# Performance work log

Hardware: AMD Instinct MI355X
Metric: run time of the kernel (lower is better)

Reference implementation:

```python
import jax, jax.numpy as jnp
import numpy as np

NUM_HEADS = 8
SPARSITY = 0.25
BOUNDARY_W = 0.5
LN_EPS = 1e-5


def setup_inputs() -> dict:
    key = jax.random.key(0)
    ks = jax.random.split(key, 16)
    B, C, H, W = 8, 256, 64, 64
    Ch = C // 4
    s = lambda *sh: 1.0 / np.sqrt(sh[-1])
    inp = {
        'x': jax.random.normal(ks[0], (B, C, H, W), jnp.float32),
        'boundary_map': jax.random.uniform(ks[1], (B, 1, H, W), jnp.float32),
        'imp_w1': jax.random.normal(ks[2], (Ch, C), jnp.float32) * s(C),
        'imp_b1': jnp.zeros((Ch,), jnp.float32),
        'imp_w2': jax.random.normal(ks[3], (1, Ch), jnp.float32) * s(Ch),
        'imp_b2': jnp.zeros((1,), jnp.float32),
        'wq': jax.random.normal(ks[4], (C, C), jnp.float32) * s(C),
        'bq': jnp.zeros((C,), jnp.float32),
        'wk': jax.random.normal(ks[5], (C, C), jnp.float32) * s(C),
        'bk': jnp.zeros((C,), jnp.float32),
        'wv': jax.random.normal(ks[6], (C, C), jnp.float32) * s(C),
        'bv': jnp.zeros((C,), jnp.float32),
        'wo': jax.random.normal(ks[7], (C, C), jnp.float32) * (0.1 * s(C)),
        'bo': jnp.zeros((C,), jnp.float32),
        'ln_g': jnp.ones((C,), jnp.float32),
        'ln_b': jnp.zeros((C,), jnp.float32),
    }
    return inp


def reference(x, boundary_map, imp_w1, imp_b1, imp_w2, imp_b2,
              wq, bq, wk, bk, wv, bv, wo, bo, ln_g, ln_b):
    B, C, H, W = x.shape
    N = H * W
    K = max(int(N * SPARSITY), 1)
    nh = NUM_HEADS
    hd = C // nh
    scale = hd ** -0.5

    # importance net: 1x1 conv -> GELU -> 1x1 conv -> sigmoid
    h = jnp.einsum('bchw,oc->bohw', x, imp_w1) + imp_b1[None, :, None, None]
    h = jax.nn.gelu(h, approximate=False)
    imp = jnp.einsum('bchw,oc->bohw', h, imp_w2) + imp_b2[None, :, None, None]
    importance = jax.nn.sigmoid(imp) + BOUNDARY_W * boundary_map  # [B,1,H,W]

    # top-K token selection
    _, top_idx = jax.lax.top_k(importance.reshape(B, N), K)  # [B,K]

    x_flat = x.transpose(0, 2, 3, 1).reshape(B, N, C)
    x_sp = jnp.take_along_axis(x_flat, top_idx[..., None], axis=1)  # [B,K,C]

    # sparse self-attention over K tokens
    q = (jnp.einsum('bkc,oc->bko', x_sp, wq) + bq).reshape(B, K, nh, hd)
    k = (jnp.einsum('bkc,oc->bko', x_sp, wk) + bk).reshape(B, K, nh, hd)
    v = (jnp.einsum('bkc,oc->bko', x_sp, wv) + bv).reshape(B, K, nh, hd)
    attn = jax.nn.softmax(jnp.einsum('bqhd,bkhd->bhqk', q, k) * scale, axis=-1)
    o = jnp.einsum('bhqk,bkhd->bqhd', attn, v).reshape(B, K, C)
    out_sp = jnp.einsum('bkc,oc->bko', o, wo) + bo

    # residual + LayerNorm
    y = out_sp + x_sp
    mu = jnp.mean(y, axis=-1, keepdims=True)
    var = jnp.mean(jnp.square(y - mu), axis=-1, keepdims=True)
    enh = (y - mu) * jax.lax.rsqrt(var + LN_EPS) * ln_g + ln_b  # [B,K,C]

    # scatter enhanced tokens back
    bidx = jnp.arange(B)[:, None]
    out_full = x_flat.at[bidx, top_idx].set(enh)
    out = out_full.reshape(B, H, W, C).transpose(0, 3, 1, 2)
    return out, importance
```

## Files before the change

kernel.cpp:

```cpp
#include <hip/hip_runtime.h>
#include <math.h>

#define B_ 8
#define C_ 256
#define N_ 4096
#define K_ 1024
#define NH_ 8
#define HD_ 32

typedef __attribute__((ext_vector_type(8))) short short8;
typedef __attribute__((ext_vector_type(8))) _Float16 half8;
typedef __attribute__((ext_vector_type(4))) _Float16 half4;
typedef __attribute__((ext_vector_type(4))) float f32x4;

#if __has_builtin(__builtin_amdgcn_exp2f)
#define EXPX(x) __builtin_amdgcn_exp2f(x)
#define QSCALE (0.17677669529663688f * 1.4426950408889634f)
#else
#define EXPX(x) __expf(x)
#define QSCALE 0.17677669529663688f
#endif

__device__ __forceinline__ unsigned bfr(float x){
  unsigned u = __float_as_uint(x);
  return (u + 0x7FFFu + ((u >> 16) & 1u)) >> 16;
}
__device__ __forceinline__ unsigned pk2(float lo, float hi){
  return bfr(lo) | (bfr(hi) << 16);
}
__device__ __forceinline__ unsigned hpk(float a, float b){
  _Float16 ha = (_Float16)a, hb = (_Float16)b;
  unsigned short ua = __builtin_bit_cast(unsigned short, ha);
  unsigned short ub = __builtin_bit_cast(unsigned short, hb);
  return (unsigned)ua | ((unsigned)ub << 16);
}
__device__ __forceinline__ half4 pk4rtz(float a, float b, float c, float d){
  auto lo = __builtin_amdgcn_cvt_pkrtz(a, b);
  auto hi = __builtin_amdgcn_cvt_pkrtz(c, d);
  uint2 u = make_uint2(__builtin_bit_cast(unsigned, lo), __builtin_bit_cast(unsigned, hi));
  return __builtin_bit_cast(half4, u);
}

__global__ __launch_bounds__(256) void w2h_kernel(
    const float* __restrict__ wq, const float* __restrict__ wk,
    const float* __restrict__ wv, const float* __restrict__ wo,
    unsigned short* __restrict__ wh)
{
  const float* src = blockIdx.y==0 ? wq : blockIdx.y==1 ? wk : blockIdx.y==2 ? wv : wo;
  const int e = (blockIdx.x*256 + threadIdx.x)*8;
  float4 a = *(const float4*)(src + e);
  float4 b = *(const float4*)(src + e + 4);
  uint4 o;
  o.x = hpk(a.x, a.y); o.y = hpk(a.z, a.w);
  o.z = hpk(b.x, b.y); o.w = hpk(b.z, b.w);
  *(uint4*)(wh + (size_t)blockIdx.y*65536 + e) = o;
}

__global__ __launch_bounds__(256) void imp_kernel(
    const float* __restrict__ x, const float* __restrict__ bmap,
    const float* __restrict__ w1, const float* __restrict__ b1,
    const float* __restrict__ w2, const float* __restrict__ b2,
    float* __restrict__ imp_out, float* __restrict__ outx)
{
  __shared__ float xs[64][256];
  const int t = threadIdx.x;
  const int b = blockIdx.x >> 6, tile = blockIdx.x & 63;
  const int n0 = tile * 64;
  {
    const int i = t & 63, cg = t >> 6;
    const float* xb = x + (size_t)b*C_*N_ + n0 + i;
    float* ox = outx + (size_t)b*C_*N_ + n0 + i;
    const int ib = (i & 15) ^ (i >> 2);
    #pragma unroll 4
    for (int cc = 0; cc < 16; cc++){
      const int c0 = cg*64 + cc*4;
      float4 v;
      v.x = xb[(size_t)(c0+0)*N_];
      v.y = xb[(size_t)(c0+1)*N_];
      v.z = xb[(size_t)(c0+2)*N_];
      v.w = xb[(size_t)(c0+3)*N_];
      *(float4*)&xs[i][4*((cg*16+cc) ^ ib)] = v;
      ox[(size_t)(c0+0)*N_] = v.x;
      ox[(size_t)(c0+1)*N_] = v.y;
      ox[(size_t)(c0+2)*N_] = v.z;
      ox[(size_t)(c0+3)*N_] = v.w;
    }
  }
  __syncthreads();
  const int pg = t & 15, og = t >> 4;
  float acc[4][4];
  #pragma unroll
  for (int pp=0;pp<4;pp++)
    #pragma unroll
    for (int oo=0;oo<4;oo++) acc[pp][oo] = 0.f;
  int pb[4];
  #pragma unroll
  for (int pp=0;pp<4;pp++){ int p = 4*pg+pp; pb[pp] = (p&15)^(p>>2); }

  float4 wa_c[4], wb_c[4];
  #pragma unroll
  for (int oo=0;oo<4;oo++){
    const float* wr = w1 + (size_t)(4*og+oo)*C_;
    wa_c[oo] = *(const float4*)wr;
    wb_c[oo] = *(const float4*)(wr+4);
  }
  #pragma unroll 2
  for (int c8 = 0; c8 < 256; c8 += 8){
    const int cn = (c8 + 8) & 255;
    float4 wa_n[4], wb_n[4];
    #pragma unroll
    for (int oo=0;oo<4;oo++){
      const float* wr = w1 + (size_t)(4*og+oo)*C_ + cn;
      wa_n[oo] = *(const float4*)wr;
      wb_n[oo] = *(const float4*)(wr+4);
    }
    const int G = c8 >> 2;
    float4 xa[4], xc[4];
    #pragma unroll
    for (int pp=0;pp<4;pp++){
      xa[pp] = *(const float4*)&xs[4*pg+pp][4*( G    ^ pb[pp])];
      xc[pp] = *(const float4*)&xs[4*pg+pp][4*((G+1) ^ pb[pp])];
    }
    #pragma unroll
    for (int pp=0;pp<4;pp++)
      #pragma unroll
      for (int oo=0;oo<4;oo++)
        acc[pp][oo] += xa[pp].x*wa_c[oo].x + xa[pp].y*wa_c[oo].y + xa[pp].z*wa_c[oo].z + xa[pp].w*wa_c[oo].w
                     + xc[pp].x*wb_c[oo].x + xc[pp].y*wb_c[oo].y + xc[pp].z*wb_c[oo].z + xc[pp].w*wb_c[oo].w;
    #pragma unroll
    for (int oo=0;oo<4;oo++){ wa_c[oo]=wa_n[oo]; wb_c[oo]=wb_n[oo]; }
  }
  float part[4] = {0.f,0.f,0.f,0.f};
  #pragma unroll
  for (int oo=0;oo<4;oo++){
    const int o = 4*og + oo;
    const float b1o = b1[o], w2o = w2[o];
    #pragma unroll
    for (int pp=0;pp<4;pp++){
      float a = acc[pp][oo] + b1o;
      float g = 0.5f*a*(1.f + erff(a*0.70710678118654752f));
      part[pp] += w2o*g;
    }
  }
  #pragma unroll
  for (int pp=0;pp<4;pp++){
    part[pp] += __shfl_xor(part[pp], 16);
    part[pp] += __shfl_xor(part[pp], 32);
  }
  __syncthreads();
  float* red = &xs[0][0];
  const int w = t >> 6;
  if ((t & 63) < 16){
    #pragma unroll
    for (int pp=0;pp<4;pp++) red[w*64 + 4*(t&15)+pp] = part[pp];
  }
  __syncthreads();
  if (t < 64){
    float s = red[t]+red[64+t]+red[128+t]+red[192+t] + b2[0];
    float sig = 1.f/(1.f+expf(-s));
    imp_out[(size_t)b*N_ + n0 + t] = sig + 0.5f*bmap[(size_t)b*N_ + n0 + t];
  }
}

__global__ __launch_bounds__(1024) void topk_kernel(const float* __restrict__ imp, int* __restrict__ tidx)
{
  __shared__ unsigned long long s[4096];
  __shared__ int ws2[16];
  const int b = blockIdx.x, t = threadIdx.x;
  const float* ib = imp + (size_t)b*N_;
  for (int m = t; m < N_; m += 1024){
    unsigned u = __float_as_uint(ib[m]);
    u = (u & 0x80000000u) ? ~u : (u | 0x80000000u);
    s[m] = ((unsigned long long)u << 32) | (unsigned)(~m);
  }
  for (int k = 2; k <= 4096; k <<= 1){
    for (int j = k >> 1; j > 0; j >>= 1){
      __syncthreads();
      #pragma unroll 2
      for (int m = t; m < 2048; m += 1024){
        int i = 2*m - (m & (j-1));
        int l = i + j;
        unsigned long long a = s[i], c = s[l];
        if ((a > c) == ((i & k) == 0)){ s[i] = c; s[l] = a; }
      }
    }
  }
  __syncthreads();
  const unsigned long long thr = s[3072];
  int sel[4]; int cnt = 0;
  #pragma unroll
  for (int u2 = 0; u2 < 4; u2++){
    const int m = 4*t + u2;
    unsigned u = __float_as_uint(ib[m]);
    u = (u & 0x80000000u) ? ~u : (u | 0x80000000u);
    unsigned long long key = ((unsigned long long)u << 32) | (unsigned)(~m);
    sel[u2] = (key >= thr) ? 1 : 0;
    cnt += sel[u2];
  }
  int incl = cnt;
  #pragma unroll
  for (int d2 = 1; d2 < 64; d2 <<= 1){
    int v2 = __shfl_up(incl, d2);
    if ((t & 63) >= d2) incl += v2;
  }
  if ((t & 63) == 63) ws2[t >> 6] = incl;
  __syncthreads();
  int base = 0;
  const int wv2 = t >> 6;
  #pragma unroll
  for (int ww = 0; ww < 16; ww++) if (ww < wv2) base += ws2[ww];
  int pos = base + incl - cnt;
  #pragma unroll
  for (int u2 = 0; u2 < 4; u2++){
    if (sel[u2]) tidx[(size_t)b*K_ + pos++] = 4*t + u2;
  }
}

__global__ __launch_bounds__(512) void qkv_kernel(
    const float* __restrict__ x, const int* __restrict__ tidx,
    const unsigned short* __restrict__ wh,
    const float* __restrict__ bq, const float* __restrict__ bk, const float* __restrict__ bv,
    float* __restrict__ xsp, unsigned short* __restrict__ qbf,
    unsigned short* __restrict__ kbf, unsigned short* __restrict__ vtb)
{
  __shared__ unsigned short xsb[16][256];
  const int t = threadIdx.x;
  const int kt = blockIdx.x, b = blockIdx.y;
  const int tok0 = kt*16;
  {
    const int i = t & 15, jg = t >> 4;
    const int n = tidx[(size_t)b*K_ + tok0 + i];
    const float* xb = x + (size_t)b*C_*N_ + n;
    float v[8];
    #pragma unroll
    for (int u = 0; u < 8; u++) v[u] = xb[(size_t)(jg*8+u)*N_];
    float* xr = xsp + ((size_t)b*K_ + tok0 + i)*C_ + jg*8;
    *(float4*)(xr)     = make_float4(v[0],v[1],v[2],v[3]);
    *(float4*)(xr + 4) = make_float4(v[4],v[5],v[6],v[7]);
    uint4 pw;
    pw.x = hpk(v[0],v[1]); pw.y = hpk(v[2],v[3]);
    pw.z = hpk(v[4],v[5]); pw.w = hpk(v[6],v[7]);
    *(uint4*)((char*)&xsb[0][0] + i*512 + ((jg ^ (i&7))*16)) = pw;
  }
  __syncthreads();

  const int lane = t & 63, w = t >> 6;
  const int g = lane >> 4, c = lane & 15;

  f32x4 acc[3][2];
  #pragma unroll
  for (int s=0;s<3;s++)
    #pragma unroll
    for (int j=0;j<2;j++) acc[s][j] = (f32x4){0.f,0.f,0.f,0.f};

  #pragma unroll 1
  for (int ks = 0; ks < 8; ks++){
    half8 Xf = *(const half8*)((const char*)&xsb[0][0] + c*512 + (((4*ks+g) ^ (c&7))*16));
    half8 Wf[3][2];
    #pragma unroll
    for (int s=0;s<3;s++)
      #pragma unroll
      for (int j=0;j<2;j++)
        Wf[s][j] = *(const half8*)(wh + (size_t)s*65536 + (32*w + 16*j + c)*C_ + ks*32 + 8*g);
    acc[0][0] = __builtin_amdgcn_mfma_f32_16x16x32_f16(Wf[0][0], Xf, acc[0][0], 0,0,0);
    acc[0][1] = __builtin_amdgcn_mfma_f32_16x16x32_f16(Wf[0][1], Xf, acc[0][1], 0,0,0);
    acc[1][0] = __builtin_amdgcn_mfma_f32_16x16x32_f16(Wf[1][0], Xf, acc[1][0], 0,0,0);
    acc[1][1] = __builtin_amdgcn_mfma_f32_16x16x32_f16(Wf[1][1], Xf, acc[1][1], 0,0,0);
    acc[2][0] = __builtin_amdgcn_mfma_f32_16x16x32_f16(Xf, Wf[2][0], acc[2][0], 0,0,0);
    acc[2][1] = __builtin_amdgcn_mfma_f32_16x16x32_f16(Xf, Wf[2][1], acc[2][1], 0,0,0);
  }

  const int bh = b*NH_ + w;
  #pragma unroll
  for (int s=0;s<2;s++){
    const float* bias = s ? bk : bq;
    const float sc = s ? 1.f : QSCALE;
    unsigned short* dstb = s ? kbf : qbf;
    #pragma unroll
    for (int j=0;j<2;j++){
      f32x4 a = acc[s][j];
      float4 bb = *(const float4*)(bias + w*32 + 16*j + 4*g);
      unsigned lo = pk2((a[0]+bb.x)*sc, (a[1]+bb.y)*sc);
      unsigned hi = pk2((a[2]+bb.z)*sc, (a[3]+bb.w)*sc);
      unsigned short* dst = dstb + ((size_t)bh*K_ + tok0 + c)*HD_ + 16*j + 4*g;
      *(uint2*)dst = make_uint2(lo, hi);
    }
  }
  const int base32 = tok0 & ~31;
  const int half   = (tok0 >> 4) & 1;
  #pragma unroll
  for (int j=0;j<2;j++){
    f32x4 a = acc[2][j];
    const float bvv = bv[w*32 + 16*j + c];
    unsigned lo = hpk(a[0]+bvv, a[1]+bvv);
    unsigned hi = hpk(a[2]+bvv, a[3]+bvv);
    unsigned short* dst = vtb + ((size_t)bh*HD_ + 16*j + c)*K_ + base32 + 8*g + 4*half;
    *(uint2*)dst = make_uint2(lo, hi);
  }
}

__global__ __launch_bounds__(512) void attn_kernel(
    const unsigned short* __restrict__ qbf, const unsigned short* __restrict__ kbf,
    const unsigned short* __restrict__ vtb, unsigned short* __restrict__ ob)
{
  __shared__ float po[4][64][19];
  const int tid = threadIdx.x;
  const int t = tid & 63, w = tid >> 6;
  const int sp = w >> 2, qq = w & 3;
  const int flat = blockIdx.x;
  const int h = flat & 7;
  const int rest = flat >> 3;
  const int qt = rest & 7;
  const int b = rest >> 3;
  const int g = t >> 4, c = t & 15;
  const int bh = b*NH_ + h;
  const int q0 = qt*128 + qq*32;

  short8 Qf0 = *(const short8*)(qbf + ((size_t)bh*K_ + q0 + c)*HD_ + g*8);
  short8 Qf1 = *(const short8*)(qbf + ((size_t)bh*K_ + q0 + 16 + c)*HD_ + g*8);

  const int kbeg = sp*512;
  const unsigned short* kp  = kbf + (size_t)bh*K_*HD_ + (size_t)(kbeg + c)*HD_ + g*8;
  const unsigned short* vp0 = vtb + ((size_t)bh*HD_ + c)*K_ + kbeg + g*8;
  const unsigned short* vp1 = vp0 + (size_t)16*K_;

  const half4 ONES = {(_Float16)1.f, (_Float16)1.f, (_Float16)1.f, (_Float16)1.f};
  f32x4 ot00 = {0.f,0.f,0.f,0.f}, ot01 = {0.f,0.f,0.f,0.f};
  f32x4 ot10 = {0.f,0.f,0.f,0.f}, ot11 = {0.f,0.f,0.f,0.f};
  f32x4 otL0 = {0.f,0.f,0.f,0.f}, otL1 = {0.f,0.f,0.f,0.f};

#define ATTN_STEP(K0c,K1c,V0c,V1c) do {                                           \
    f32x4 z = {0.f,0.f,0.f,0.f};                                                  \
    __builtin_amdgcn_s_setprio(1);                                                \
    f32x4 s00 = __builtin_amdgcn_mfma_f32_16x16x32_bf16(K0c, Qf0, z, 0, 0, 0);    \
    f32x4 s01 = __builtin_amdgcn_mfma_f32_16x16x32_bf16(K1c, Qf0, z, 0, 0, 0);    \
    f32x4 s10 = __builtin_amdgcn_mfma_f32_16x16x32_bf16(K0c, Qf1, z, 0, 0, 0);    \
    f32x4 s11 = __builtin_amdgcn_mfma_f32_16x16x32_bf16(K1c, Qf1, z, 0, 0, 0);    \
    __builtin_amdgcn_s_setprio(0);                                                \
    float p00[4], p01[4], p10[4], p11[4];                                         \
    _Pragma("unroll")                                                             \
    for (int r=0;r<4;r++){                                                        \
      p00[r] = EXPX(s00[r]); p01[r] = EXPX(s01[r]);                               \
      p10[r] = EXPX(s10[r]); p11[r] = EXPX(s11[r]);                               \
    }                                                                             \
    half4 P00 = pk4rtz(p00[0], p00[1], p00[2], p00[3]);                           \
    half4 P01 = pk4rtz(p01[0], p01[1], p01[2], p01[3]);                           \
    half4 P10 = pk4rtz(p10[0], p10[1], p10[2], p10[3]);                           \
    half4 P11 = pk4rtz(p11[0], p11[1], p11[2], p11[3]);                           \
    half4 A0lo = __builtin_shufflevector(V0c, V0c, 0, 1, 2, 3);                   \
    half4 A0hi = __builtin_shufflevector(V0c, V0c, 4, 5, 6, 7);                   \
    half4 A1lo = __builtin_shufflevector(V1c, V1c, 0, 1, 2, 3);                   \
    half4 A1hi = __builtin_shufflevector(V1c, V1c, 4, 5, 6, 7);                   \
    __builtin_amdgcn_s_setprio(1);                                                \
    ot00 = __builtin_amdgcn_mfma_f32_16x16x16f16(A0lo, P00, ot00, 0, 0, 0);       \
    ot00 = __builtin_amdgcn_mfma_f32_16x16x16f16(A0hi, P01, ot00, 0, 0, 0);       \
    ot01 = __builtin_amdgcn_mfma_f32_16x16x16f16(A1lo, P00, ot01, 0, 0, 0);       \
    ot01 = __builtin_amdgcn_mfma_f32_16x16x16f16(A1hi, P01, ot01, 0, 0, 0);       \
    ot10 = __builtin_amdgcn_mfma_f32_16x16x16f16(A0lo, P10, ot10, 0, 0, 0);       \
    ot10 = __builtin_amdgcn_mfma_f32_16x16x16f16(A0hi, P11, ot10, 0, 0, 0);       \
    ot11 = __builtin_amdgcn_mfma_f32_16x16x16f16(A1lo, P10, ot11, 0, 0, 0);       \
    ot11 = __builtin_amdgcn_mfma_f32_16x16x16f16(A1hi, P11, ot11, 0, 0, 0);       \
    otL0 = __builtin_amdgcn_mfma_f32_16x16x16f16(ONES, P00, otL0, 0, 0, 0);       \
    otL0 = __builtin_amdgcn_mfma_f32_16x16x16f16(ONES, P01, otL0, 0, 0, 0);       \
    otL1 = __builtin_amdgcn_mfma_f32_16x16x16f16(ONES, P10, otL1, 0, 0, 0);       \
    otL1 = __builtin_amdgcn_mfma_f32_16x16x16f16(ONES, P11, otL1, 0, 0, 0);       \
    __builtin_amdgcn_s_setprio(0);                                                \
  } while(0)

  short8 K0a = *(const short8*)(kp);
  short8 K1a = *(const short8*)(kp + 16*HD_);
  half8  V0a = *(const half8*)(vp0);
  half8  V1a = *(const half8*)(vp1);
  kp += 32*HD_; vp0 += 32; vp1 += 32;
  short8 K0b = *(const short8*)(kp);
  short8 K1b = *(const short8*)(kp + 16*HD_);
  half8  V0b = *(const half8*)(vp0);
  half8  V1b = *(const half8*)(vp1);

  for (int it = 0; it < 16; it += 2){
    kp += 32*HD_; vp0 += 32; vp1 += 32;
    short8 K0n = *(const short8*)(kp);
    short8 K1n = *(const short8*)(kp + 16*HD_);
    half8  V0n = *(const half8*)(vp0);
    half8  V1n = *(const half8*)(vp1);
    ATTN_STEP(K0a, K1a, V0a, V1a);
    K0a = K0n; K1a = K1n; V0a = V0n; V1a = V1n;
    kp += 32*HD_; vp0 += 32; vp1 += 32;
    short8 K0m = *(const short8*)(kp);
    short8 K1m = *(const short8*)(kp + 16*HD_);
    half8  V0m = *(const half8*)(vp0);
    half8  V1m = *(const half8*)(vp1);
    ATTN_STEP(K0b, K1b, V0b, V1b);
    K0b = K0m; K1b = K1m; V0b = V0m; V1b = V1m;
  }
#undef ATTN_STEP

  if (sp == 1){
    float* d = po[qq][t];
    d[0]=ot00[0]; d[1]=ot00[1]; d[2]=ot00[2];  d[3]=ot00[3];
    d[4]=ot01[0]; d[5]=ot01[1]; d[6]=ot01[2];  d[7]=ot01[3];
    d[8]=ot10[0]; d[9]=ot10[1]; d[10]=ot10[2]; d[11]=ot10[3];
    d[12]=ot11[0];d[13]=ot11[1];d[14]=ot11[2]; d[15]=ot11[3];
    d[16]=otL0[0]; d[17]=otL1[0];
  }
  __syncthreads();
  if (sp == 0){
    const float* d = po[qq][t];
    ot00[0]+=d[0]; ot00[1]+=d[1]; ot00[2]+=d[2];  ot00[3]+=d[3];
    ot01[0]+=d[4]; ot01[1]+=d[5]; ot01[2]+=d[6];  ot01[3]+=d[7];
    ot10[0]+=d[8]; ot10[1]+=d[9]; ot10[2]+=d[10]; ot10[3]+=d[11];
    ot11[0]+=d[12];ot11[1]+=d[13];ot11[2]+=d[14]; ot11[3]+=d[15];
    const float L0 = otL0[0] + d[16];
    const float L1 = otL1[0] + d[17];
    const float i0 = 1.f / L0, i1 = 1.f / L1;
    unsigned short* o0 = ob + ((size_t)b*K_ + q0 + c)*C_ + h*HD_;
    unsigned short* o1 = ob + ((size_t)b*K_ + q0 + 16 + c)*C_ + h*HD_;
    *(uint2*)(o0 + 4*g)      = make_uint2(hpk(ot00[0]*i0, ot00[1]*i0), hpk(ot00[2]*i0, ot00[3]*i0));
    *(uint2*)(o0 + 16 + 4*g) = make_uint2(hpk(ot01[0]*i0, ot01[1]*i0), hpk(ot01[2]*i0, ot01[3]*i0));
    *(uint2*)(o1 + 4*g)      = make_uint2(hpk(ot10[0]*i1, ot10[1]*i1), hpk(ot10[2]*i1, ot10[3]*i1));
    *(uint2*)(o1 + 16 + 4*g) = make_uint2(hpk(ot11[0]*i1, ot11[1]*i1), hpk(ot11[2]*i1, ot11[3]*i1));
  }
}

__global__ __launch_bounds__(512) void out_kernel(
    const unsigned short* __restrict__ ob, const float* __restrict__ xsp,
    const int* __restrict__ tidx, const unsigned short* __restrict__ woh, const float* __restrict__ bo,
    const float* __restrict__ lng, const float* __restrict__ lnb,
    float* __restrict__ out)
{
  __shared__ float red1[8][32], red2[8][32];
  __shared__ float mus[32], rss[32];
  __shared__ int nn[32];
  const int t = threadIdx.x;
  const int kt = blockIdx.x, b = blockIdx.y;
  const int tok0 = kt*32;
  const int lane = t & 63, w = t >> 6;
  const int g = lane >> 4, c = lane & 15;

  if (t < 32) nn[t] = tidx[(size_t)b*K_ + tok0 + t];

  f32x4 acc[2][2];
  #pragma unroll
  for (int j=0;j<2;j++)
    #pragma unroll
    for (int tt=0;tt<2;tt++) acc[j][tt] = (f32x4){0.f,0.f,0.f,0.f};

  const unsigned short* ob0 = ob + ((size_t)b*K_ + tok0)*C_;
  const unsigned short* wr0 = woh + (32*w + c)*C_;

  #pragma unroll 1
  for (int ks = 0; ks < 8; ks++){
    half8 Wf0 = *(const half8*)(wr0 + ks*32 + 8*g);
    half8 Wf1 = *(const half8*)(wr0 + 16*C_ + ks*32 + 8*g);
    #pragma unroll
    for (int tt=0;tt<2;tt++){
      half8 Of = *(const half8*)(ob0 + (size_t)(16*tt + c)*C_ + ks*32 + 8*g);
      acc[0][tt] = __builtin_amdgcn_mfma_f32_16x16x32_f16(Wf0, Of, acc[0][tt], 0,0,0);
      acc[1][tt] = __builtin_amdgcn_mfma_f32_16x16x32_f16(Wf1, Of, acc[1][tt], 0,0,0);
    }
  }

  float4 bb[2];
  #pragma unroll
  for (int j=0;j<2;j++) bb[j] = *(const float4*)(bo + 32*w + 16*j + 4*g);
  #pragma unroll
  for (int tt=0;tt<2;tt++){
    const float* xr = xsp + ((size_t)b*K_ + tok0 + 16*tt + c)*C_ + 32*w + 4*g;
    #pragma unroll
    for (int j=0;j<2;j++){
      float4 xv = *(const float4*)(xr + 16*j);
      acc[j][tt][0] += bb[j].x + xv.x;
      acc[j][tt][1] += bb[j].y + xv.y;
      acc[j][tt][2] += bb[j].z + xv.z;
      acc[j][tt][3] += bb[j].w + xv.w;
    }
  }

  #pragma unroll
  for (int tt=0;tt<2;tt++){
    float s1 = 0.f, s2 = 0.f;
    #pragma unroll
    for (int j=0;j<2;j++)
      #pragma unroll
      for (int r=0;r<4;r++){ float y = acc[j][tt][r]; s1 += y; s2 += y*y; }
    s1 += __shfl_xor(s1, 16); s2 += __shfl_xor(s2, 16);
    s1 += __shfl_xor(s1, 32); s2 += __shfl_xor(s2, 32);
    if (g == 0){ red1[w][16*tt + c] = s1; red2[w][16*tt + c] = s2; }
  }
  __syncthreads();
  if (t < 32){
    float a = 0.f, q2 = 0.f;
    #pragma unroll
    for (int ww=0;ww<8;ww++){ a += red1[ww][t]; q2 += red2[ww][t]; }
    float mu = a*(1.f/256.f);
    float var = q2*(1.f/256.f) - mu*mu;
    mus[t] = mu;
    rss[t] = rsqrtf(var + 1e-5f);
  }
  __syncthreads();

  float4 gv[2], bv2[2];
  #pragma unroll
  for (int j=0;j<2;j++){
    gv[j]  = *(const float4*)(lng + 32*w + 16*j + 4*g);
    bv2[j] = *(const float4*)(lnb + 32*w + 16*j + 4*g);
  }
  float* outb = out + (size_t)b*C_*N_;
  #pragma unroll
  for (int tt=0;tt<2;tt++){
    const int tok = 16*tt + c;
    const float mu = mus[tok], rs = rss[tok];
    const int n = nn[tok];
    #pragma unroll
    for (int j=0;j<2;j++){
      const int oc0 = 32*w + 16*j + 4*g;
      const float* gvp = (const float*)&gv[j];
      const float* bvp = (const float*)&bv2[j];
      #pragma unroll
      for (int r=0;r<4;r++)
        outb[(size_t)(oc0 + r)*N_ + n] = (acc[j][tt][r]-mu)*rs*gvp[r] + bvp[r];
    }
  }
}

extern "C" void kernel_launch(void* const* d_in, const int* in_sizes, int n_in,
                              void* d_out, int out_size, void* d_ws, size_t ws_size,
                              hipStream_t stream)
{
  const float* x    = (const float*)d_in[0];
  const float* bmap = (const float*)d_in[1];
  const float* w1   = (const float*)d_in[2];
  const float* b1   = (const float*)d_in[3];
  const float* w2   = (const float*)d_in[4];
  const float* b2   = (const float*)d_in[5];
  const float* wq   = (const float*)d_in[6];
  const float* bq   = (const float*)d_in[7];
  const float* wk   = (const float*)d_in[8];
  const float* bk   = (const float*)d_in[9];
  const float* wv   = (const float*)d_in[10];
  const float* bv   = (const float*)d_in[11];
  const float* wo   = (const float*)d_in[12];
  const float* bo   = (const float*)d_in[13];
  const float* lng  = (const float*)d_in[14];
  const float* lnb  = (const float*)d_in[15];

  float* out = (float*)d_out;
  float* imp_out = out + (size_t)B_*C_*N_;

  char* wsb = (char*)d_ws;
  int*   tidx = (int*)wsb;
  float* xsp  = (float*)(wsb + 65536);
  unsigned short* ob16 = (unsigned short*)(xsp + (size_t)B_*K_*C_);
  unsigned short* qbf = ob16 + 2*(size_t)B_*K_*C_;
  unsigned short* kbf = qbf + (size_t)B_*NH_*K_*HD_;
  unsigned short* vtb = kbf + (size_t)B_*NH_*K_*HD_;
  unsigned short* wh  = vtb + (size_t)B_*NH_*K_*HD_;

  w2h_kernel <<<dim3(32, 4),    dim3(256),  0, stream>>>(wq, wk, wv, wo, wh);
  imp_kernel <<<dim3(512),      dim3(256),  0, stream>>>(x, bmap, w1, b1, w2, b2, imp_out, out);
  topk_kernel<<<dim3(8),        dim3(1024), 0, stream>>>(imp_out, tidx);
  qkv_kernel <<<dim3(64, 8),    dim3(512),  0, stream>>>(x, tidx, wh, bq, bk, bv, xsp, qbf, kbf, vtb);
  attn_kernel<<<dim3(512),      dim3(512),  0, stream>>>(qbf, kbf, vtb, ob16);
  out_kernel <<<dim3(32, 8),    dim3(512),  0, stream>>>(ob16, xsp, tidx, wh + 3*65536, bo, lng, lnb, out);
}
```

Measured before the change: 147.7 us.

## Drop LDS staging in importance kernel, read x directly from global per thread

The importance kernel no longer stages a 64x256 x tile in shared memory. Each thread now reads float4 columns of x straight from global memory (served by L1/L2), and only the og==0 threads write the copy to outx. This removes the 64KB LDS footprint and a barrier, which may raise occupancy. The cost is 16 redundant global reads of each x element per block and the loss of the register-prefetch pipelining of weights.

```diff
diff --git a/kernel.cpp b/kernel.cpp
--- a/kernel.cpp
+++ b/kernel.cpp
@@ -62,73 +62,51 @@
     const float* __restrict__ w2, const float* __restrict__ b2,
     float* __restrict__ imp_out, float* __restrict__ outx)
 {
-  __shared__ float xs[64][256];
+  __shared__ float red[4][64];
   const int t = threadIdx.x;
   const int b = blockIdx.x >> 6, tile = blockIdx.x & 63;
   const int n0 = tile * 64;
-  {
-    const int i = t & 63, cg = t >> 6;
-    const float* xb = x + (size_t)b*C_*N_ + n0 + i;
-    float* ox = outx + (size_t)b*C_*N_ + n0 + i;
-    const int ib = (i & 15) ^ (i >> 2);
-    #pragma unroll 4
-    for (int cc = 0; cc < 16; cc++){
-      const int c0 = cg*64 + cc*4;
-      float4 v;
-      v.x = xb[(size_t)(c0+0)*N_];
-      v.y = xb[(size_t)(c0+1)*N_];
-      v.z = xb[(size_t)(c0+2)*N_];
-      v.w = xb[(size_t)(c0+3)*N_];
-      *(float4*)&xs[i][4*((cg*16+cc) ^ ib)] = v;
-      ox[(size_t)(c0+0)*N_] = v.x;
-      ox[(size_t)(c0+1)*N_] = v.y;
-      ox[(size_t)(c0+2)*N_] = v.z;
-      ox[(size_t)(c0+3)*N_] = v.w;
-    }
-  }
-  __syncthreads();
-  const int pg = t & 15, og = t >> 4;
+  const int p4 = t & 15, og = t >> 4;
+  const float* xb = x + (size_t)b*C_*N_ + n0 + 4*p4;
+  float* ox = outx + (size_t)b*C_*N_ + n0 + 4*p4;
+  const float* wr0 = w1 + (size_t)(4*og+0)*C_;
+  const float* wr1 = w1 + (size_t)(4*og+1)*C_;
+  const float* wr2 = w1 + (size_t)(4*og+2)*C_;
+  const float* wr3 = w1 + (size_t)(4*og+3)*C_;
+
   float acc[4][4];
   #pragma unroll
   for (int pp=0;pp<4;pp++)
     #pragma unroll
     for (int oo=0;oo<4;oo++) acc[pp][oo] = 0.f;
-  int pb[4];
-  #pragma unroll
-  for (int pp=0;pp<4;pp++){ int p = 4*pg+pp; pb[pp] = (p&15)^(p>>2); }
-
-  float4 wa_c[4], wb_c[4];
-  #pragma unroll
-  for (int oo=0;oo<4;oo++){
-    const float* wr = w1 + (size_t)(4*og+oo)*C_;
-    wa_c[oo] = *(const float4*)wr;
-    wb_c[oo] = *(const float4*)(wr+4);
-  }
+
   #pragma unroll 2
-  for (int c8 = 0; c8 < 256; c8 += 8){
-    const int cn = (c8 + 8) & 255;
-    float4 wa_n[4], wb_n[4];
-    #pragma unroll
-    for (int oo=0;oo<4;oo++){
-      const float* wr = w1 + (size_t)(4*og+oo)*C_ + cn;
-      wa_n[oo] = *(const float4*)wr;
-      wb_n[oo] = *(const float4*)(wr+4);
-    }
-    const int G = c8 >> 2;
-    float4 xa[4], xc[4];
-    #pragma unroll
-    for (int pp=0;pp<4;pp++){
-      xa[pp] = *(const float4*)&xs[4*pg+pp][4*( G    ^ pb[pp])];
-      xc[pp] = *(const float4*)&xs[4*pg+pp][4*((G+1) ^ pb[pp])];
-    }
+  for (int c = 0; c < 256; c += 4){
+    float4 xv0 = *(const float4*)(xb + (size_t)(c+0)*N_);
+    float4 xv1 = *(const float4*)(xb + (size_t)(c+1)*N_);
+    float4 xv2 = *(const float4*)(xb + (size_t)(c+2)*N_);
+    float4 xv3 = *(const float4*)(xb + (size_t)(c+3)*N_);
+    float4 wv0 = *(const float4*)(wr0 + c);
+    float4 wv1 = *(const float4*)(wr1 + c);
+    float4 wv2 = *(const float4*)(wr2 + c);
+    float4 wv3 = *(const float4*)(wr3 + c);
+    if (og == 0){
+      *(float4*)(ox + (size_t)(c+0)*N_) = xv0;
+      *(float4*)(ox + (size_t)(c+1)*N_) = xv1;
+      *(float4*)(ox + (size_t)(c+2)*N_) = xv2;
+      *(float4*)(ox + (size_t)(c+3)*N_) = xv3;
+    }
+    const float xp0[4] = {xv0.x, xv0.y, xv0.z, xv0.w};
+    const float xp1[4] = {xv1.x, xv1.y, xv1.z, xv1.w};
+    const float xp2[4] = {xv2.x, xv2.y, xv2.z, xv2.w};
+    const float xp3[4] = {xv3.x, xv3.y, xv3.z, xv3.w};
+    const float4 wv[4] = {wv0, wv1, wv2, wv3};
     #pragma unroll
     for (int pp=0;pp<4;pp++)
       #pragma unroll
       for (int oo=0;oo<4;oo++)
-        acc[pp][oo] += xa[pp].x*wa_c[oo].x + xa[pp].y*wa_c[oo].y + xa[pp].z*wa_c[oo].z + xa[pp].w*wa_c[oo].w
-                     + xc[pp].x*wb_c[oo].x + xc[pp].y*wb_c[oo].y + xc[pp].z*wb_c[oo].z + xc[pp].w*wb_c[oo].w;
-    #pragma unroll
-    for (int oo=0;oo<4;oo++){ wa_c[oo]=wa_n[oo]; wb_c[oo]=wb_n[oo]; }
+        acc[pp][oo] += xp0[pp]*wv[oo].x + xp1[pp]*wv[oo].y
+                     + xp2[pp]*wv[oo].z + xp3[pp]*wv[oo].w;
   }
   float part[4] = {0.f,0.f,0.f,0.f};
   #pragma unroll
@@ -147,16 +125,14 @@
     part[pp] += __shfl_xor(part[pp], 16);
     part[pp] += __shfl_xor(part[pp], 32);
   }
-  __syncthreads();
-  float* red = &xs[0][0];
   const int w = t >> 6;
   if ((t & 63) < 16){
     #pragma unroll
-    for (int pp=0;pp<4;pp++) red[w*64 + 4*(t&15)+pp] = part[pp];
+    for (int pp=0;pp<4;pp++) red[w][4*(t&15)+pp] = part[pp];
   }
   __syncthreads();
   if (t < 64){
-    float s = red[t]+red[64+t]+red[128+t]+red[192+t] + b2[0];
+    float s = red[0][t]+red[1][t]+red[2][t]+red[3][t] + b2[0];
     float sig = 1.f/(1.f+expf(-s));
     imp_out[(size_t)b*N_ + n0 + t] = sig + 0.5f*bmap[(size_t)b*N_ + n0 + t];
   }
```

New measurement: 164.8 us. 11.5% more time.
